# Kernel optimization log

Hardware: AMD Instinct MI355X
Metric: run time of the kernel (lower is better)

The kernel has to match this reference:

```python
import jax, jax.numpy as jnp
import numpy as np

VOCAB = 1024   # must equal HID (embedding Linear consumes vocab-sized x)
HID = 1024
EMB = 256
NOS = 12
B, M = 512, 8
TEMP = 1.0


def setup_inputs() -> dict:
    key = jax.random.key(0)
    ks = jax.random.split(key, 12)
    N = B * M
    target = jax.random.normal(ks[0], (B, M, HID), jnp.float32)
    # precomputed standard Gumbel noise per step (training=True path)
    u = jax.random.uniform(ks[1], (NOS, N, VOCAB), jnp.float32, 1e-6, 1.0 - 1e-6)
    gumbels = -jnp.log(-jnp.log(u))
    sh = 1.0 / np.sqrt(HID)
    sv = 1.0 / np.sqrt(VOCAB)
    sos = 0.01 * jax.random.normal(ks[2], (EMB,), jnp.float32)
    W_ih = jax.random.uniform(ks[3], (HID, EMB), jnp.float32, -sh, sh)
    b_ih = jax.random.uniform(ks[4], (HID,), jnp.float32, -sh, sh)
    W_hh = jax.random.uniform(ks[5], (HID, HID), jnp.float32, -sh, sh)
    b_hh = jax.random.uniform(ks[6], (HID,), jnp.float32, -sh, sh)
    W_out = jax.random.uniform(ks[7], (VOCAB, HID), jnp.float32, -sh, sh)
    b_out = jax.random.uniform(ks[8], (VOCAB,), jnp.float32, -sh, sh)
    W_emb = jax.random.uniform(ks[9], (EMB, VOCAB), jnp.float32, -sv, sv)
    b_emb = jax.random.uniform(ks[10], (EMB,), jnp.float32, -sv, sv)
    return dict(target=target, gumbels=gumbels, sos=sos,
                W_ih=W_ih, b_ih=b_ih, W_hh=W_hh, b_hh=b_hh,
                W_out=W_out, b_out=b_out, W_emb=W_emb, b_emb=b_emb)


def reference(target, gumbels, sos, W_ih, b_ih, W_hh, b_hh, W_out, b_out, W_emb, b_emb):
    b_, m_, h_ = target.shape
    prev = target.reshape(b_ * m_, h_)            # [N, HID]
    e0 = jnp.broadcast_to(sos, (prev.shape[0], sos.shape[0]))  # [N, EMB]

    def step(carry, g):
        prev_h, e = carry
        h = jnp.tanh(e @ W_ih.T + b_ih + prev_h @ W_hh.T + b_hh)   # RNNCell
        logits = h @ W_out.T + b_out                               # [N, VOCAB]
        x = jax.nn.softmax((logits + g) / TEMP, axis=-1)           # gumbel-softmax
        e_next = x @ W_emb.T + b_emb                               # [N, EMB]
        return (h, e_next), x

    _, xs = jax.lax.scan(step, (prev, e0), gumbels)  # xs: [NOS, N, VOCAB]
    return jnp.transpose(xs, (1, 0, 2))              # [N, NOS, VOCAB]
```

## Files before the change

### kernel.cpp

```cpp
#include <hip/hip_runtime.h>

#define N_TOT 4096
#define HIDN  1024
#define EMBD  256
#define VOC   1024
#define NSTEP 12

typedef __bf16 bf16;
typedef _Float16 h16;
typedef __bf16 bf16x8 __attribute__((ext_vector_type(8)));
typedef __bf16 bf16x4 __attribute__((ext_vector_type(4)));
typedef _Float16 h16x8 __attribute__((ext_vector_type(8)));
typedef float  f32x4  __attribute__((ext_vector_type(4)));

#define VMCNT(n) asm volatile("s_waitcnt vmcnt(" #n ")" ::: "memory")
#define MEMFENCE() asm volatile("" ::: "memory")

static __device__ __forceinline__ f32x4 mfma16(bf16x8 a, bf16x8 b, f32x4 c) {
  return __builtin_amdgcn_mfma_f32_16x16x32_bf16(a, b, c, 0, 0, 0);
}

static __device__ __forceinline__ float fast_tanh(float x) {
  float e = __expf(2.0f * x);
  return 1.0f - 2.0f / (e + 1.0f);
}

static __device__ __forceinline__ void gload16(const bf16* g, bf16* l) {
  __builtin_amdgcn_global_load_lds(
      (const __attribute__((address_space(1))) void*)g,
      (__attribute__((address_space(3))) void*)l, 16, 0, 0);
}


__global__ void prep_kernel(const float* __restrict__ Wih, const float* __restrict__ Whh,
                            const float* __restrict__ Wout, const float* __restrict__ Wemb,
                            const float* __restrict__ target, const float* __restrict__ sos,
                            const float* __restrict__ bih, const float* __restrict__ bhh,
                            bf16* __restrict__ wih_b, bf16* __restrict__ whh_b,
                            bf16* __restrict__ wout_b, bf16* __restrict__ wemb_b,
                            bf16* __restrict__ hbuf, bf16* __restrict__ ebuf,
                            float* __restrict__ bias1) {
  for (int q = blockIdx.x * blockDim.x + threadIdx.x; q < 1966336;
       q += blockDim.x * gridDim.x) {
    if (q < 1703936) {
      const float* s; bf16* d; int o;
      if (q < 65536)        { s = Wih;    d = wih_b;  o = q; }
      else if (q < 327680)  { s = Whh;    d = whh_b;  o = q - 65536; }
      else if (q < 589824)  { s = Wout;   d = wout_b; o = q - 327680; }
      else if (q < 655360)  { s = Wemb;   d = wemb_b; o = q - 589824; }
      else                  { s = target; d = hbuf;   o = q - 655360; }
      f32x4 v = *(const f32x4*)&s[(size_t)o * 4];
      bf16x4 b; b[0] = (bf16)v.x; b[1] = (bf16)v.y; b[2] = (bf16)v.z; b[3] = (bf16)v.w;
      *(bf16x4*)&d[(size_t)o * 4] = b;
    } else if (q < 1966080) {
      int o = q - 1703936;
      f32x4 v = *(const f32x4*)&sos[(o & 63) * 4];
      bf16x4 b; b[0] = (bf16)v.x; b[1] = (bf16)v.y; b[2] = (bf16)v.z; b[3] = (bf16)v.w;
      *(bf16x4*)&ebuf[(size_t)o * 4] = b;
    } else {
      int o = q - 1966080;
      f32x4 a = *(const f32x4*)&bih[o * 4];
      f32x4 c = *(const f32x4*)&bhh[o * 4];
      f32x4 r; r.x = a.x + c.x; r.y = a.y + c.y; r.z = a.z + c.z; r.w = a.w + c.w;
      *(f32x4*)&bias1[o * 4] = r;
    }
  }
}


template <bool TWO, int NT>
static __device__ __forceinline__ void pipe_gemm(
    const bf16* __restrict__ A0, const bf16* __restrict__ B0, int K0,
    const bf16* __restrict__ A1, const bf16* __restrict__ B1, int K1,
    bf16* lds, int m0, int n0, int w, int lane, f32x4 acc[4][2])
{
  const int wr = w >> 1, wc = w & 1;
  const int lr = lane & 15, lk = lane >> 4;
  const int srow = lane >> 3;
  const int scol = (((lane & 7) ^ srow) << 3);

  auto stage = [&](int t, int bsel) {
    const bf16 *A, *B; int K, k0;
    if (TWO && t < 4) { A = A0; B = B0; K = K0; k0 = t << 6; }
    else if (TWO)     { A = A1; B = B1; K = K1; k0 = (t - 4) << 6; }
    else              { A = A0; B = B0; K = K0; k0 = t << 6; }
    bf16* base = lds + bsel * 12288;
#pragma unroll
    for (int r = 0; r < 4; ++r)
      gload16(&A[(size_t)(m0 + w * 32 + r * 8 + srow) * K + k0 + scol],
              base + (w * 32 + r * 8) * 64);
#pragma unroll
    for (int r = 0; r < 2; ++r)
      gload16(&B[(size_t)(n0 + w * 16 + r * 8 + srow) * K + k0 + scol],
              base + 8192 + (w * 16 + r * 8) * 64);
  };

  stage(0, 0); stage(1, 1);
  VMCNT(6);
  MEMFENCE();
  __builtin_amdgcn_s_barrier();
  MEMFENCE();
  for (int t = 0; t < NT; ++t) {
    if (t + 2 < NT) stage(t + 2, (t + 2) % 3);
    const bf16* Ab = lds + (t % 3) * 12288;
    const bf16* Bb = Ab + 8192;
    __builtin_amdgcn_s_setprio(1);
#pragma unroll
    for (int kk = 0; kk < 2; ++kk) {
      bf16x8 af[4], bfr[2];
#pragma unroll
      for (int mi = 0; mi < 4; ++mi) {
        int row = wr * 64 + mi * 16 + lr;
        af[mi] = *(const bf16x8*)&Ab[row * 64 + ((((kk << 2) | lk) ^ (row & 7)) << 3)];
      }
#pragma unroll
      for (int ni = 0; ni < 2; ++ni) {
        int row = wc * 32 + ni * 16 + lr;
        bfr[ni] = *(const bf16x8*)&Bb[row * 64 + ((((kk << 2) | lk) ^ (row & 7)) << 3)];
      }
#pragma unroll
      for (int mi = 0; mi < 4; ++mi)
#pragma unroll
        for (int ni = 0; ni < 2; ++ni)
          acc[mi][ni] = mfma16(af[mi], bfr[ni], acc[mi][ni]);
    }
    __builtin_amdgcn_s_setprio(0);
    if (t < NT - 2)       VMCNT(6);
    else if (t == NT - 2) VMCNT(0);
    MEMFENCE();
    __builtin_amdgcn_s_barrier();
    MEMFENCE();
  }
}


__global__ __launch_bounds__(256, 2)
void rnn_cell_kernel(const bf16* __restrict__ e,
                     const bf16* __restrict__ hprev,
                     const bf16* __restrict__ Wih,
                     const bf16* __restrict__ Whh,
                     const float* __restrict__ bias,
                     bf16* __restrict__ hnew)
{
  __shared__ bf16 lds[3 * 12288];
  const int tid = threadIdx.x;
  const int lane = tid & 63;
  const int w = tid >> 6;
  const int wr = w >> 1, wc = w & 1;
  const int id = (blockIdx.x & 7) * 64 + (blockIdx.x >> 3);
  const int m0 = (id >> 4) * 128;
  const int n0 = (id & 15) * 64;
  const int lr = lane & 15, lk = lane >> 4;

  f32x4 acc[4][2] = {};
  pipe_gemm<true, 20>(e, Wih, EMBD, hprev, Whh, HIDN, lds, m0, n0, w, lane, acc);

#pragma unroll
  for (int mi = 0; mi < 4; ++mi) {
    int rowb = m0 + wr * 64 + mi * 16 + lk * 4;
#pragma unroll
    for (int ni = 0; ni < 2; ++ni) {
      int col = n0 + wc * 32 + ni * 16 + lr;
      float bs = bias[col];
#pragma unroll
      for (int j = 0; j < 4; ++j)
        hnew[(size_t)(rowb + j) * HIDN + col] = (bf16)fast_tanh(acc[mi][ni][j] + bs);
    }
  }
}


__global__ __launch_bounds__(256, 2)
void logits_kernel(const bf16* __restrict__ h,
                   const bf16* __restrict__ Wout,
                   const float* __restrict__ bout,
                   h16* __restrict__ lbuf)
{
  __shared__ bf16 lds[3 * 12288];
  const int tid = threadIdx.x;
  const int lane = tid & 63;
  const int w = tid >> 6;
  const int wr = w >> 1, wc = w & 1;
  const int id = (blockIdx.x & 7) * 64 + (blockIdx.x >> 3);
  const int m0 = (id >> 4) * 128;
  const int n0 = (id & 15) * 64;
  const int lr = lane & 15, lk = lane >> 4;

  f32x4 acc[4][2] = {};
  pipe_gemm<false, 16>(h, Wout, HIDN, nullptr, nullptr, 0, lds, m0, n0, w, lane, acc);

#pragma unroll
  for (int mi = 0; mi < 4; ++mi) {
    int rowb = m0 + wr * 64 + mi * 16 + lk * 4;
#pragma unroll
    for (int ni = 0; ni < 2; ++ni) {
      int col = n0 + wc * 32 + ni * 16 + lr;
      float bs = bout[col];
#pragma unroll
      for (int j = 0; j < 4; ++j) {
        int row = rowb + j;
        lbuf[(size_t)row * VOC + col] = (h16)(acc[mi][ni][j] + bs);
      }
    }
  }
}


__global__ __launch_bounds__(1024)
void softmax_emb_kernel(const h16* __restrict__ lbuf,
                        const float* __restrict__ gum,
                        const bf16* __restrict__ Wemb,
                        const float* __restrict__ bemb,
                        float* __restrict__ out,
                        bf16* __restrict__ enext,
                        int step)
{
  __shared__ bf16 xs[16 * 1032];
  const int tid = threadIdx.x;
  const int lane = tid & 63;
  const int w = tid >> 6;
  const int n0 = blockIdx.x * 16;

  {
    int r = w;
    const h16* lrow = lbuf + (size_t)(n0 + r) * VOC;
    const float* grow = gum + (size_t)(n0 + r) * VOC;
    float s[16];
    float m = -1e30f;
#pragma unroll
    for (int i = 0; i < 2; ++i) {
      h16x8 lv = *(const h16x8*)&lrow[i * 512 + lane * 8];
      f32x4 g0 = *(const f32x4*)&grow[i * 512 + lane * 8];
      f32x4 g1 = *(const f32x4*)&grow[i * 512 + lane * 8 + 4];
#pragma unroll
      for (int j = 0; j < 4; ++j) {
        float f0 = (float)lv[j] + g0[j];
        float f1 = (float)lv[4 + j] + g1[j];
        s[i * 8 + j] = f0; s[i * 8 + 4 + j] = f1;
        m = fmaxf(m, fmaxf(f0, f1));
      }
    }
#pragma unroll
    for (int off = 32; off; off >>= 1) m = fmaxf(m, __shfl_xor(m, off));
    float sum = 0.f;
#pragma unroll
    for (int i = 0; i < 16; ++i) { s[i] = __expf(s[i] - m); sum += s[i]; }
#pragma unroll
    for (int off = 32; off; off >>= 1) sum += __shfl_xor(sum, off);
    float inv = 1.0f / sum;
    float* orow = out + ((size_t)(n0 + r) * NSTEP + step) * VOC;
#pragma unroll
    for (int i = 0; i < 2; ++i) {
      f32x4 v0, v1;
      bf16x8 bv;
#pragma unroll
      for (int j = 0; j < 4; ++j) {
        float x0 = s[i * 8 + j] * inv;
        float x1 = s[i * 8 + 4 + j] * inv;
        v0[j] = x0; v1[j] = x1;
        bv[j] = (bf16)x0; bv[4 + j] = (bf16)x1;
      }
      *(f32x4*)&orow[i * 512 + lane * 8] = v0;
      *(f32x4*)&orow[i * 512 + lane * 8 + 4] = v1;
      *(bf16x8*)&xs[r * 1032 + i * 512 + lane * 8] = bv;
    }
  }
  __syncthreads();

  const int lr = lane & 15, lk = lane >> 4;
  f32x4 acc = {};
  const int col = w * 16 + lr;
  for (int k0 = 0; k0 < VOC; k0 += 32) {
    bf16x8 a = *(bf16x8*)&xs[lr * 1032 + k0 + lk * 8];
    bf16x8 b = *(const bf16x8*)&Wemb[(size_t)col * VOC + k0 + lk * 8];
    acc = mfma16(a, b, acc);
  }
  float bb = bemb[col];
#pragma unroll
  for (int j = 0; j < 4; ++j) {
    int n = n0 + lk * 4 + j;
    enext[(size_t)n * EMBD + col] = (bf16)(acc[j] + bb);
  }
}


extern "C" void kernel_launch(void* const* d_in, const int* in_sizes, int n_in,
                              void* d_out, int out_size, void* d_ws, size_t ws_size,
                              hipStream_t stream) {
  const float* target  = (const float*)d_in[0];
  const float* gumbels = (const float*)d_in[1];
  const float* sos     = (const float*)d_in[2];
  const float* W_ih    = (const float*)d_in[3];
  const float* b_ih    = (const float*)d_in[4];
  const float* W_hh    = (const float*)d_in[5];
  const float* b_hh    = (const float*)d_in[6];
  const float* W_out   = (const float*)d_in[7];
  const float* b_out   = (const float*)d_in[8];
  const float* W_emb   = (const float*)d_in[9];
  const float* b_emb   = (const float*)d_in[10];
  float* out = (float*)d_out;

  char* ws = (char*)d_ws;
  bf16* wih_b  = (bf16*)(ws);
  bf16* whh_b  = (bf16*)(ws + (1u << 20));
  bf16* wout_b = (bf16*)(ws + (3u << 20));
  bf16* wemb_b = (bf16*)(ws + (5u << 20));
  float* bias1 = (float*)(ws + (6u << 20));
  bf16* hbuf0  = (bf16*)(ws + (7u << 20));
  bf16* hbuf1  = (bf16*)(ws + (15u << 20));
  bf16* ebuf   = (bf16*)(ws + (23u << 20));
  h16*  lbuf   = (h16*) (ws + (25u << 20));

  prep_kernel<<<2048, 256, 0, stream>>>(W_ih, W_hh, W_out, W_emb, target, sos,
                                        b_ih, b_hh, wih_b, whh_b, wout_b, wemb_b,
                                        hbuf0, ebuf, bias1);

  bf16* hb[2] = {hbuf0, hbuf1};
  for (int t = 0; t < NSTEP; ++t) {
    bf16* hp = hb[t & 1];
    bf16* hn = hb[(t + 1) & 1];
    rnn_cell_kernel<<<(N_TOT / 128) * (HIDN / 64), 256, 0, stream>>>(
        ebuf, hp, wih_b, whh_b, bias1, hn);
    logits_kernel<<<(N_TOT / 128) * (VOC / 64), 256, 0, stream>>>(
        hn, wout_b, b_out, lbuf);
    softmax_emb_kernel<<<N_TOT / 16, 1024, 0, stream>>>(
        lbuf, gumbels + (size_t)t * N_TOT * VOC, wemb_b, b_emb, out, ebuf, t);
  }
}
```

Before: 649.0 us.

## Fuse logits GEMM, gumbel-softmax and embedding GEMM into one kernel

```diff
diff --git a/kernel.cpp b/kernel.cpp
--- a/kernel.cpp
+++ b/kernel.cpp
@@ -7,10 +7,8 @@
 #define NSTEP 12
 
 typedef __bf16 bf16;
-typedef _Float16 h16;
 typedef __bf16 bf16x8 __attribute__((ext_vector_type(8)));
 typedef __bf16 bf16x4 __attribute__((ext_vector_type(4)));
-typedef _Float16 h16x8 __attribute__((ext_vector_type(8)));
 typedef float  f32x4  __attribute__((ext_vector_type(4)));
 
 #define VMCNT(n) asm volatile("s_waitcnt vmcnt(" #n ")" ::: "memory")
@@ -170,116 +168,153 @@
 }
 
 
-__global__ __launch_bounds__(256, 2)
-void logits_kernel(const bf16* __restrict__ h,
-                   const bf16* __restrict__ Wout,
-                   const float* __restrict__ bout,
-                   h16* __restrict__ lbuf)
+__global__ __launch_bounds__(512)
+void logits_sm_emb_kernel(const bf16* __restrict__ h,
+                          const float* __restrict__ gum,
+                          const bf16* __restrict__ Wout,
+                          const float* __restrict__ bout,
+                          const bf16* __restrict__ Wemb,
+                          const float* __restrict__ bemb,
+                          float* __restrict__ out,
+                          bf16* __restrict__ enext,
+                          int step)
 {
-  __shared__ bf16 lds[3 * 12288];
+  __shared__ bf16 hx[16 * 1024];
+  __shared__ float pmax[128];
+  __shared__ float psum[128];
   const int tid = threadIdx.x;
   const int lane = tid & 63;
   const int w = tid >> 6;
-  const int wr = w >> 1, wc = w & 1;
-  const int id = (blockIdx.x & 7) * 64 + (blockIdx.x >> 3);
-  const int m0 = (id >> 4) * 128;
-  const int n0 = (id & 15) * 64;
   const int lr = lane & 15, lk = lane >> 4;
-
-  f32x4 acc[4][2] = {};
-  pipe_gemm<false, 16>(h, Wout, HIDN, nullptr, nullptr, 0, lds, m0, n0, w, lane, acc);
-
-#pragma unroll
-  for (int mi = 0; mi < 4; ++mi) {
-    int rowb = m0 + wr * 64 + mi * 16 + lk * 4;
-#pragma unroll
-    for (int ni = 0; ni < 2; ++ni) {
-      int col = n0 + wc * 32 + ni * 16 + lr;
-      float bs = bout[col];
-#pragma unroll
-      for (int j = 0; j < 4; ++j) {
-        int row = rowb + j;
-        lbuf[(size_t)row * VOC + col] = (h16)(acc[mi][ni][j] + bs);
+  const int r0 = blockIdx.x * 16;
+
+#pragma unroll
+  for (int i = 0; i < 4; ++i) {
+    int hr = w + i * 8;
+    int row = hr >> 1, half = hr & 1;
+    gload16(&h[(size_t)(r0 + row) * HIDN + (half * 64 + (lane ^ (row & 7))) * 8],
+            hx + row * 1024 + half * 512);
+  }
+  VMCNT(0);
+  __syncthreads();
+
+  f32x4 acc[8] = {};
+  {
+    const bf16* wp = Wout + (size_t)(w * 128 + lr) * HIDN + lk * 8;
+    bf16x8 b0[8], b1[8];
+#pragma unroll
+    for (int ni = 0; ni < 8; ++ni)
+      b0[ni] = *(const bf16x8*)(wp + ni * 16 * HIDN);
+    for (int kt = 0; kt < 32; kt += 2) {
+#pragma unroll
+      for (int ni = 0; ni < 8; ++ni)
+        b1[ni] = *(const bf16x8*)(wp + ni * 16 * HIDN + (kt + 1) * 32);
+      bf16x8 af0 = *(const bf16x8*)&hx[lr * 1024 + (((kt * 4 + lk) ^ (lr & 7)) << 3)];
+#pragma unroll
+      for (int ni = 0; ni < 8; ++ni)
+        acc[ni] = mfma16(af0, b0[ni], acc[ni]);
+      if (kt + 2 < 32) {
+#pragma unroll
+        for (int ni = 0; ni < 8; ++ni)
+          b0[ni] = *(const bf16x8*)(wp + ni * 16 * HIDN + (kt + 2) * 32);
       }
-    }
-  }
-}
-
-
-__global__ __launch_bounds__(1024)
-void softmax_emb_kernel(const h16* __restrict__ lbuf,
-                        const float* __restrict__ gum,
-                        const bf16* __restrict__ Wemb,
-                        const float* __restrict__ bemb,
-                        float* __restrict__ out,
-                        bf16* __restrict__ enext,
-                        int step)
-{
-  __shared__ bf16 xs[16 * 1032];
-  const int tid = threadIdx.x;
-  const int lane = tid & 63;
-  const int w = tid >> 6;
-  const int n0 = blockIdx.x * 16;
-
+      bf16x8 af1 = *(const bf16x8*)&hx[lr * 1024 + ((((kt + 1) * 4 + lk) ^ (lr & 7)) << 3)];
+#pragma unroll
+      for (int ni = 0; ni < 8; ++ni)
+        acc[ni] = mfma16(af1, b1[ni], acc[ni]);
+    }
+  }
+
+  float vals[8][4];
+#pragma unroll
+  for (int ni = 0; ni < 8; ++ni) {
+    int col = w * 128 + ni * 16 + lr;
+    float bo = bout[col];
+#pragma unroll
+    for (int j = 0; j < 4; ++j)
+      vals[ni][j] = acc[ni][j] + bo + gum[(size_t)(r0 + lk * 4 + j) * VOC + col];
+  }
+  float mx[4];
+#pragma unroll
+  for (int j = 0; j < 4; ++j) {
+    float m = vals[0][j];
+#pragma unroll
+    for (int ni = 1; ni < 8; ++ni) m = fmaxf(m, vals[ni][j]);
+    m = fmaxf(m, __shfl_xor(m, 1)); m = fmaxf(m, __shfl_xor(m, 2));
+    m = fmaxf(m, __shfl_xor(m, 4)); m = fmaxf(m, __shfl_xor(m, 8));
+    mx[j] = m;
+  }
+  if (lr == 0) {
+#pragma unroll
+    for (int j = 0; j < 4; ++j) pmax[(lk * 4 + j) * 8 + w] = mx[j];
+  }
+  __syncthreads();
+#pragma unroll
+  for (int j = 0; j < 4; ++j) {
+    int row = lk * 4 + j;
+    float m = pmax[row * 8];
+#pragma unroll
+    for (int q = 1; q < 8; ++q) m = fmaxf(m, pmax[row * 8 + q]);
+    mx[j] = m;
+  }
+  float sm[4] = {0.f, 0.f, 0.f, 0.f};
+#pragma unroll
+  for (int ni = 0; ni < 8; ++ni)
+#pragma unroll
+    for (int j = 0; j < 4; ++j) {
+      vals[ni][j] = __expf(vals[ni][j] - mx[j]);
+      sm[j] += vals[ni][j];
+    }
+#pragma unroll
+  for (int j = 0; j < 4; ++j) {
+    sm[j] += __shfl_xor(sm[j], 1); sm[j] += __shfl_xor(sm[j], 2);
+    sm[j] += __shfl_xor(sm[j], 4); sm[j] += __shfl_xor(sm[j], 8);
+  }
+  if (lr == 0) {
+#pragma unroll
+    for (int j = 0; j < 4; ++j) psum[(lk * 4 + j) * 8 + w] = sm[j];
+  }
+  __syncthreads();
+  float inv[4];
+#pragma unroll
+  for (int j = 0; j < 4; ++j) {
+    int row = lk * 4 + j;
+    float s = psum[row * 8];
+#pragma unroll
+    for (int q = 1; q < 8; ++q) s += psum[row * 8 + q];
+    inv[j] = 1.0f / s;
+  }
+
+#pragma unroll
+  for (int ni = 0; ni < 8; ++ni) {
+    int col = w * 128 + ni * 16 + lr;
+    int chunk = col >> 3, cin = col & 7;
+#pragma unroll
+    for (int j = 0; j < 4; ++j) {
+      int row = lk * 4 + j;
+      float p = vals[ni][j] * inv[j];
+      out[((size_t)(r0 + row) * NSTEP + step) * VOC + col] = p;
+      hx[row * 1024 + ((chunk ^ (row & 7)) << 3) + cin] = (bf16)p;
+    }
+  }
+  __syncthreads();
+
+  f32x4 acc2[2] = {};
   {
-    int r = w;
-    const h16* lrow = lbuf + (size_t)(n0 + r) * VOC;
-    const float* grow = gum + (size_t)(n0 + r) * VOC;
-    float s[16];
-    float m = -1e30f;
-#pragma unroll
-    for (int i = 0; i < 2; ++i) {
-      h16x8 lv = *(const h16x8*)&lrow[i * 512 + lane * 8];
-      f32x4 g0 = *(const f32x4*)&grow[i * 512 + lane * 8];
-      f32x4 g1 = *(const f32x4*)&grow[i * 512 + lane * 8 + 4];
-#pragma unroll
-      for (int j = 0; j < 4; ++j) {
-        float f0 = (float)lv[j] + g0[j];
-        float f1 = (float)lv[4 + j] + g1[j];
-        s[i * 8 + j] = f0; s[i * 8 + 4 + j] = f1;
-        m = fmaxf(m, fmaxf(f0, f1));
-      }
-    }
-#pragma unroll
-    for (int off = 32; off; off >>= 1) m = fmaxf(m, __shfl_xor(m, off));
-    float sum = 0.f;
-#pragma unroll
-    for (int i = 0; i < 16; ++i) { s[i] = __expf(s[i] - m); sum += s[i]; }
-#pragma unroll
-    for (int off = 32; off; off >>= 1) sum += __shfl_xor(sum, off);
-    float inv = 1.0f / sum;
-    float* orow = out + ((size_t)(n0 + r) * NSTEP + step) * VOC;
-#pragma unroll
-    for (int i = 0; i < 2; ++i) {
-      f32x4 v0, v1;
-      bf16x8 bv;
-#pragma unroll
-      for (int j = 0; j < 4; ++j) {
-        float x0 = s[i * 8 + j] * inv;
-        float x1 = s[i * 8 + 4 + j] * inv;
-        v0[j] = x0; v1[j] = x1;
-        bv[j] = (bf16)x0; bv[4 + j] = (bf16)x1;
-      }
-      *(f32x4*)&orow[i * 512 + lane * 8] = v0;
-      *(f32x4*)&orow[i * 512 + lane * 8 + 4] = v1;
-      *(bf16x8*)&xs[r * 1032 + i * 512 + lane * 8] = bv;
-    }
-  }
-  __syncthreads();
-
-  const int lr = lane & 15, lk = lane >> 4;
-  f32x4 acc = {};
-  const int col = w * 16 + lr;
-  for (int k0 = 0; k0 < VOC; k0 += 32) {
-    bf16x8 a = *(bf16x8*)&xs[lr * 1032 + k0 + lk * 8];
-    bf16x8 b = *(const bf16x8*)&Wemb[(size_t)col * VOC + k0 + lk * 8];
-    acc = mfma16(a, b, acc);
-  }
-  float bb = bemb[col];
-#pragma unroll
-  for (int j = 0; j < 4; ++j) {
-    int n = n0 + lk * 4 + j;
-    enext[(size_t)n * EMBD + col] = (bf16)(acc[j] + bb);
+    const bf16* wep = Wemb + (size_t)(w * 32 + lr) * VOC + lk * 8;
+    for (int kt = 0; kt < 32; ++kt) {
+      bf16x8 af = *(const bf16x8*)&hx[lr * 1024 + (((kt * 4 + lk) ^ (lr & 7)) << 3)];
+      acc2[0] = mfma16(af, *(const bf16x8*)(wep + kt * 32), acc2[0]);
+      acc2[1] = mfma16(af, *(const bf16x8*)(wep + 16 * VOC + kt * 32), acc2[1]);
+    }
+  }
+#pragma unroll
+  for (int ni = 0; ni < 2; ++ni) {
+    int col = w * 32 + ni * 16 + lr;
+    float bb = bemb[col];
+#pragma unroll
+    for (int j = 0; j < 4; ++j)
+      enext[(size_t)(r0 + lk * 4 + j) * EMBD + col] = (bf16)(acc2[ni][j] + bb);
   }
 }
 
@@ -309,7 +344,6 @@
   bf16* hbuf0  = (bf16*)(ws + (7u << 20));
   bf16* hbuf1  = (bf16*)(ws + (15u << 20));
   bf16* ebuf   = (bf16*)(ws + (23u << 20));
-  h16*  lbuf   = (h16*) (ws + (25u << 20));
 
   prep_kernel<<<2048, 256, 0, stream>>>(W_ih, W_hh, W_out, W_emb, target, sos,
                                         b_ih, b_hh, wih_b, whh_b, wout_b, wemb_b,
@@ -321,9 +355,8 @@
     bf16* hn = hb[(t + 1) & 1];
     rnn_cell_kernel<<<(N_TOT / 128) * (HIDN / 64), 256, 0, stream>>>(
         ebuf, hp, wih_b, whh_b, bias1, hn);
-    logits_kernel<<<(N_TOT / 128) * (VOC / 64), 256, 0, stream>>>(
-        hn, wout_b, b_out, lbuf);
-    softmax_emb_kernel<<<N_TOT / 16, 1024, 0, stream>>>(
-        lbuf, gumbels + (size_t)t * N_TOT * VOC, wemb_b, b_emb, out, ebuf, t);
-  }
-}
+    logits_sm_emb_kernel<<<N_TOT / 16, 512, 0, stream>>>(
+        hn, gumbels + (size_t)t * N_TOT * VOC, wout_b, b_out, wemb_b, b_emb,
+        out, ebuf, t);
+  }
+}
```

Result: slower. 1.172 ms (+80.6%).
